# Performance work log

Measured on AMD Instinct MI355X. Metric: run time of the kernel, lower is better.

The kernel has to match this reference:

```python
import jax, jax.numpy as jnp
import numpy as np

NUM_HEADS = 32

def setup_inputs() -> dict:
    key = jax.random.key(0)
    k1, k2, k3 = jax.random.split(key, 3)
    B, C, H, W = 4, 768, 32, 32
    x = jax.random.normal(k1, (B, C, H, W), dtype=jnp.float32)
    # 1x1 conv kernels represented as [C_in, C_out] matrices
    w_qkv = jax.random.normal(k2, (C, 3 * C), dtype=jnp.float32) * (2.0 / (3 * C)) ** 0.5
    b_qkv = jnp.zeros((3 * C,), dtype=jnp.float32)
    w_proj = jax.random.normal(k3, (C, C), dtype=jnp.float32) * (2.0 / C) ** 0.5
    b_proj = jnp.zeros((C,), dtype=jnp.float32)
    return {"x": x, "w_qkv": w_qkv, "b_qkv": b_qkv, "w_proj": w_proj, "b_proj": b_proj}

def reference(x, w_qkv, b_qkv, w_proj, b_proj):
    B, C, H, W = x.shape
    h = NUM_HEADS
    hd = C // h
    scale = hd ** (-0.5)
    # qkv 1x1 conv (channels_first): [B,C,H,W] -> [B,3C,H,W]
    qkv = jnp.einsum('bchw,cd->bdhw', x, w_qkv) + b_qkv[None, :, None, None]
    qkv = qkv.reshape(B, 3, h, hd, H * W)
    q = qkv[:, 0]  # [B,h,hd,HW]
    k = qkv[:, 1]  # [B,h,hd,HW]
    v = qkv[:, 2]  # [B,h,hd,HW]
    # attn = q^T @ k : [B,h,HW,HW]
    attn = jnp.einsum('bhdq,bhdk->bhqk', q, k) * scale
    attn = jax.nn.softmax(attn, axis=-1)
    # out = (attn @ v^T)^T : [B,h,hd,HW]
    o = jnp.einsum('bhqk,bhdk->bhdq', attn, v)
    o = o.reshape(B, C, H, W)
    # proj 1x1 conv
    out = jnp.einsum('bchw,cf->bfhw', o, w_proj) + b_proj[None, :, None, None]
    return out
```

## Files before the change

kernel.cpp:

```cpp
#include <hip/hip_runtime.h>
#include <hip/hip_bf16.h>

#define B_  4
#define C_  768
#define N_  1024
#define NH  32
#define HD  24
#define HDP 32
#define D3  2304
#define QSCALE 0.29448889f

typedef __hip_bfloat16 bf16;
typedef __attribute__((ext_vector_type(8))) short bf16x8;
typedef __attribute__((ext_vector_type(4))) float f32x4;

__device__ __forceinline__ unsigned cvt_pk_bf16(float lo, float hi) {
    unsigned r;
    asm volatile("v_cvt_pk_bf16_f32 %0, %1, %2" : "=v"(r) : "v"(lo), "v"(hi));
    return r;
}

__device__ __forceinline__ float fast_exp2(float x) {
    float r;
    asm volatile("v_exp_f32 %0, %1" : "=v"(r) : "v"(x));
    return r;
}

__device__ __forceinline__ void gload_lds16(const bf16* g, bf16* l) {
    __builtin_amdgcn_global_load_lds(
        (const __attribute__((address_space(1))) void*)g,
        (__attribute__((address_space(3))) void*)l, 16, 0, 0);
}

__global__ __launch_bounds__(256) void transpose_cvt(
        const float* __restrict__ in, bf16* __restrict__ out,
        int R, int Cc, long inb, long outb) {
    __shared__ float tile[32][33];
    const int b = blockIdx.z;
    const float* src = in + (size_t)b * inb;
    bf16* dst = out + (size_t)b * outb;
    const int r0 = blockIdx.y * 32, c0 = blockIdx.x * 32;
    const int tx = threadIdx.x, ty = threadIdx.y;
    #pragma unroll
    for (int k = 0; k < 4; k++)
        tile[ty + 8*k][tx] = src[(size_t)(r0 + ty + 8*k) * Cc + c0 + tx];
    __syncthreads();
    #pragma unroll
    for (int k = 0; k < 4; k++)
        dst[(size_t)(c0 + ty + 8*k) * R + r0 + tx] = __float2bfloat16(tile[tx][ty + 8*k]);
}

__global__ __launch_bounds__(256) void fill_ones(bf16* __restrict__ vB) {
    bf16* row = vB + ((size_t)blockIdx.x * HDP + 24) * N_;
    const ushort4 ones = {0x3F80, 0x3F80, 0x3F80, 0x3F80};
    *(ushort4*)&row[threadIdx.x * 4] = ones;
}

__global__ __launch_bounds__(256) void gemm_qkv(
        const bf16* __restrict__ xt, const bf16* __restrict__ wqT,
        const float* __restrict__ bqkv,
        bf16* __restrict__ qT, bf16* __restrict__ kT, bf16* __restrict__ vB) {
    __shared__ bf16 As[2][128 * 32];
    __shared__ bf16 Bs[2][128 * 32];

    const int b = blockIdx.z;
    const bool vmode = (blockIdx.y >= 12);
    const bf16* Ap; const bf16* Bp; int M0, Nc0;
    if (!vmode) {
        Ap = xt + (size_t)b * N_ * C_;  Bp = wqT;
        M0 = blockIdx.x * 128;          Nc0 = blockIdx.y * 128;
    } else {
        Ap = wqT + (size_t)1536 * C_;   Bp = xt + (size_t)b * N_ * C_;
        M0 = (blockIdx.y - 12) * 128;   Nc0 = blockIdx.x * 128;
    }

    const int t = threadIdx.x;
    const int lane = t & 63, wid = t >> 6;
    const int c = lane & 15, g = lane >> 4;
    const int wm = wid >> 1, wn = wid & 1;

    const int srow = lane >> 2, schunk = lane & 3;
    const bf16* Ag0 = Ap + (size_t)(M0 + wid * 32 + srow) * C_ + schunk * 8;
    const bf16* Ag1 = Ag0 + 16 * C_;
    const bf16* Bg0 = Bp + (size_t)(Nc0 + wid * 32 + srow) * C_ + schunk * 8;
    const bf16* Bg1 = Bg0 + 16 * C_;

    f32x4 acc[4][4];
    #pragma unroll
    for (int i = 0; i < 4; i++)
        #pragma unroll
        for (int j = 0; j < 4; j++) acc[i][j] = f32x4{0.f, 0.f, 0.f, 0.f};

    gload_lds16(Ag0, &As[0][(wid * 32) * 32]);
    gload_lds16(Ag1, &As[0][(wid * 32 + 16) * 32]);
    gload_lds16(Bg0, &Bs[0][(wid * 32) * 32]);
    gload_lds16(Bg1, &Bs[0][(wid * 32 + 16) * 32]);
    __syncthreads();

    int cur = 0;
    for (int s = 0; s < 24; s++) {
        if (s < 23) {
            const int k1 = (s + 1) * 32;
            gload_lds16(Ag0 + k1, &As[cur ^ 1][(wid * 32) * 32]);
            gload_lds16(Ag1 + k1, &As[cur ^ 1][(wid * 32 + 16) * 32]);
            gload_lds16(Bg0 + k1, &Bs[cur ^ 1][(wid * 32) * 32]);
            gload_lds16(Bg1 + k1, &Bs[cur ^ 1][(wid * 32 + 16) * 32]);
        }
        bf16x8 af[4], bfr[4];
        #pragma unroll
        for (int mi = 0; mi < 4; mi++)
            af[mi] = *(const bf16x8*)&As[cur][(wm * 64 + mi * 16 + c) * 32 + g * 8];
        #pragma unroll
        for (int ni = 0; ni < 4; ni++)
            bfr[ni] = *(const bf16x8*)&Bs[cur][(wn * 64 + ni * 16 + c) * 32 + g * 8];
        #pragma unroll
        for (int mi = 0; mi < 4; mi++)
            #pragma unroll
            for (int ni = 0; ni < 4; ni++)
                acc[mi][ni] = __builtin_amdgcn_mfma_f32_16x16x32_bf16(
                    af[mi], bfr[ni], acc[mi][ni], 0, 0, 0);
        __syncthreads();
        cur ^= 1;
    }

    const int row0 = M0 + wm * 64, col0 = Nc0 + wn * 64;
    if (!vmode) {
        #pragma unroll
        for (int ni = 0; ni < 4; ni++) {
            const int j = col0 + ni * 16 + c;
            const int issec = j >= 768;
            bf16* dstbase = issec ? kT : qT;
            const int dd = j - (issec ? 768 : 0);
            const int hh = dd / 24, hd = dd % 24;
            const float bq = bqkv[j];
            const float sca = issec ? 1.0f : QSCALE;
            #pragma unroll
            for (int mi = 0; mi < 4; mi++)
                #pragma unroll
                for (int r = 0; r < 4; r++) {
                    const int n = row0 + mi * 16 + 4 * g + r;
                    dstbase[(((size_t)(b * NH + hh) * N_) + n) * HDP + hd] =
                        __float2bfloat16((acc[mi][ni][r] + bq) * sca);
                }
        }
    } else {
        #pragma unroll
        for (int mi = 0; mi < 4; mi++)
            #pragma unroll
            for (int r = 0; r < 4; r++) {
                const int vd = row0 + mi * 16 + 4 * g + r;
                const int hh = vd / 24, hd = vd % 24;
                const float bq = bqkv[1536 + vd];
                #pragma unroll
                for (int ni = 0; ni < 4; ni++) {
                    const int n = col0 + ni * 16 + c;
                    vB[((size_t)(b * NH + hh) * HDP + hd) * N_ + n] =
                        __float2bfloat16(acc[mi][ni][r] + bq);
                }
            }
    }
}

__global__ __launch_bounds__(256) void gemm_proj(
        const bf16* __restrict__ wpT, const bf16* __restrict__ obuf,
        const float* __restrict__ bproj, float* __restrict__ outF) {
    __shared__ bf16 As[2][64 * 32];
    __shared__ bf16 Bs[2][128 * 32];

    const int b = blockIdx.z;
    const bf16* Ap = wpT;
    const bf16* Bp = obuf + (size_t)b * N_ * C_;
    const int M0 = blockIdx.x * 64, Nc0 = blockIdx.y * 128;

    const int t = threadIdx.x;
    const int lane = t & 63, wid = t >> 6;
    const int c = lane & 15, g = lane >> 4;
    const int wm = wid >> 1, wn = wid & 1;

    const int srow = lane >> 2, schunk = lane & 3;
    const bf16* AgP = Ap + (size_t)(M0 + wid * 16 + srow) * C_ + schunk * 8;
    const bf16* Bg0 = Bp + (size_t)(Nc0 + wid * 32 + srow) * C_ + schunk * 8;
    const bf16* Bg1 = Bg0 + 16 * C_;

    f32x4 acc[2][4];
    #pragma unroll
    for (int i = 0; i < 2; i++)
        #pragma unroll
        for (int j = 0; j < 4; j++) acc[i][j] = f32x4{0.f, 0.f, 0.f, 0.f};

    gload_lds16(AgP, &As[0][(wid * 16) * 32]);
    gload_lds16(Bg0, &Bs[0][(wid * 32) * 32]);
    gload_lds16(Bg1, &Bs[0][(wid * 32 + 16) * 32]);
    __syncthreads();

    int cur = 0;
    for (int s = 0; s < 24; s++) {
        if (s < 23) {
            const int k1 = (s + 1) * 32;
            gload_lds16(AgP + k1, &As[cur ^ 1][(wid * 16) * 32]);
            gload_lds16(Bg0 + k1, &Bs[cur ^ 1][(wid * 32) * 32]);
            gload_lds16(Bg1 + k1, &Bs[cur ^ 1][(wid * 32 + 16) * 32]);
        }
        bf16x8 af[2], bfr[4];
        #pragma unroll
        for (int mi = 0; mi < 2; mi++)
            af[mi] = *(const bf16x8*)&As[cur][(wm * 32 + mi * 16 + c) * 32 + g * 8];
        #pragma unroll
        for (int ni = 0; ni < 4; ni++)
            bfr[ni] = *(const bf16x8*)&Bs[cur][(wn * 64 + ni * 16 + c) * 32 + g * 8];
        #pragma unroll
        for (int mi = 0; mi < 2; mi++)
            #pragma unroll
            for (int ni = 0; ni < 4; ni++)
                acc[mi][ni] = __builtin_amdgcn_mfma_f32_16x16x32_bf16(
                    af[mi], bfr[ni], acc[mi][ni], 0, 0, 0);
        __syncthreads();
        cur ^= 1;
    }

    const int row0 = M0 + wm * 32, col0 = Nc0 + wn * 64;
    #pragma unroll
    for (int mi = 0; mi < 2; mi++)
        #pragma unroll
        for (int r = 0; r < 4; r++) {
            const int f = row0 + mi * 16 + 4 * g + r;
            const float bp = bproj[f];
            #pragma unroll
            for (int ni = 0; ni < 4; ni++) {
                const int n = col0 + ni * 16 + c;
                outF[((size_t)b * C_ + f) * N_ + n] = acc[mi][ni][r] + bp;
            }
        }
}

__global__ __launch_bounds__(256) void attn_mfma(
        const bf16* __restrict__ qT, const bf16* __restrict__ kT,
        const bf16* __restrict__ vB, bf16* __restrict__ obuf) {
    __shared__ bf16 Kb[2][64 * 40];
    __shared__ bf16 Vb[2][32 * 72];
    __shared__ bf16 Ps[4][32 * 72];

    const int t = threadIdx.x, lane = t & 63, wid = t >> 6;
    const int c = lane & 15, g = lane >> 4;
    const int bid = blockIdx.x;
    const int xcd = bid & 7, idx = bid >> 3;
    const int hl = xcd * 16 + (idx & 15);
    const int qb = idx >> 4;
    const int b = hl >> 5, h = hl & 31;
    const int q0 = qb * 128 + wid * 32;
    const size_t hb = (size_t)(b * NH + h);
    const bf16* qh = qT + hb * N_ * HDP;
    const bf16* kh = kT + hb * N_ * HDP;
    const bf16* vh = vB + hb * HDP * N_;
    bf16* myPs = &Ps[wid][0];

    const bf16x8 qf0 = *(const bf16x8*)(qh + (size_t)(q0 + c) * HDP + g * 8);
    const bf16x8 qf1 = *(const bf16x8*)(qh + (size_t)(q0 + 16 + c) * HDP + g * 8);
    f32x4 o00 = {0.f,0.f,0.f,0.f}, o01 = {0.f,0.f,0.f,0.f};
    f32x4 o10 = {0.f,0.f,0.f,0.f}, o11 = {0.f,0.f,0.f,0.f};

    const bf16* kgp = kh + (size_t)(t >> 2) * HDP + (t & 3) * 8;
    const bf16* vgp = vh + (size_t)(t >> 3) * N_ + (t & 7) * 8;
    const int kws = (t >> 2) * 40 + (t & 3) * 8;
    const int vws = (t >> 3) * 72 + (t & 7) * 8;

    int4 rk = *(const int4*)kgp;
    int4 rv = *(const int4*)vgp;
    *(int4*)&Kb[0][kws] = rk;
    *(int4*)&Vb[0][vws] = rv;
    __syncthreads();

    int cur = 0;
    for (int kt = 0; kt < 16; kt++) {
        if (kt < 15) {
            const int k1 = (kt + 1) * 64;
            rk = *(const int4*)(kgp + (size_t)k1 * HDP);
            rv = *(const int4*)(vgp + k1);
        }
        f32x4 st0[4], st1[4];
        #pragma unroll
        for (int tt = 0; tt < 4; tt++) {
            bf16x8 kf = *(const bf16x8*)&Kb[cur][(tt * 16 + c) * 40 + g * 8];
            f32x4 z = {0.f, 0.f, 0.f, 0.f};
            st0[tt] = __builtin_amdgcn_mfma_f32_16x16x32_bf16(kf, qf0, z, 0, 0, 0);
            st1[tt] = __builtin_amdgcn_mfma_f32_16x16x32_bf16(kf, qf1, z, 0, 0, 0);
        }
        float p0[16], p1[16];
        #pragma unroll
        for (int tt = 0; tt < 4; tt++)
            #pragma unroll
            for (int r = 0; r < 4; r++) {
                p0[tt * 4 + r] = fast_exp2(st0[tt][r]);
                p1[tt * 4 + r] = fast_exp2(st1[tt][r]);
            }
        #pragma unroll
        for (int tt = 0; tt < 4; tt++) {
            uint2 w0, w1;
            w0.x = cvt_pk_bf16(p0[tt * 4 + 0], p0[tt * 4 + 1]);
            w0.y = cvt_pk_bf16(p0[tt * 4 + 2], p0[tt * 4 + 3]);
            w1.x = cvt_pk_bf16(p1[tt * 4 + 0], p1[tt * 4 + 1]);
            w1.y = cvt_pk_bf16(p1[tt * 4 + 2], p1[tt * 4 + 3]);
            *(uint2*)&myPs[c * 72 + tt * 16 + g * 4]        = w0;
            *(uint2*)&myPs[(16 + c) * 72 + tt * 16 + g * 4] = w1;
        }
        bf16x8 pa00 = *(const bf16x8*)&myPs[c * 72 + g * 8];
        bf16x8 pa01 = *(const bf16x8*)&myPs[c * 72 + 32 + g * 8];
        bf16x8 pa10 = *(const bf16x8*)&myPs[(16 + c) * 72 + g * 8];
        bf16x8 pa11 = *(const bf16x8*)&myPs[(16 + c) * 72 + 32 + g * 8];

        bf16x8 va0 = *(const bf16x8*)&Vb[cur][c * 72 + g * 8];
        bf16x8 va1 = *(const bf16x8*)&Vb[cur][c * 72 + 32 + g * 8];
        bf16x8 vb0 = *(const bf16x8*)&Vb[cur][(16 + c) * 72 + g * 8];
        bf16x8 vb1 = *(const bf16x8*)&Vb[cur][(16 + c) * 72 + 32 + g * 8];
        o00 = __builtin_amdgcn_mfma_f32_16x16x32_bf16(pa00, va0, o00, 0, 0, 0);
        o00 = __builtin_amdgcn_mfma_f32_16x16x32_bf16(pa01, va1, o00, 0, 0, 0);
        o01 = __builtin_amdgcn_mfma_f32_16x16x32_bf16(pa00, vb0, o01, 0, 0, 0);
        o01 = __builtin_amdgcn_mfma_f32_16x16x32_bf16(pa01, vb1, o01, 0, 0, 0);
        o10 = __builtin_amdgcn_mfma_f32_16x16x32_bf16(pa10, va0, o10, 0, 0, 0);
        o10 = __builtin_amdgcn_mfma_f32_16x16x32_bf16(pa11, va1, o10, 0, 0, 0);
        o11 = __builtin_amdgcn_mfma_f32_16x16x32_bf16(pa10, vb0, o11, 0, 0, 0);
        o11 = __builtin_amdgcn_mfma_f32_16x16x32_bf16(pa11, vb1, o11, 0, 0, 0);

        if (kt < 15) {
            *(int4*)&Kb[cur ^ 1][kws] = rk;
            *(int4*)&Vb[cur ^ 1][vws] = rv;
        }
        __syncthreads();
        cur ^= 1;
    }

    float inv0[4], inv1[4];
    #pragma unroll
    for (int r = 0; r < 4; r++) {
        inv0[r] = 1.f / __shfl(o01[r], g * 16 + 8);
        inv1[r] = 1.f / __shfl(o11[r], g * 16 + 8);
    }
    #pragma unroll
    for (int dt = 0; dt < 2; dt++) {
        const int dcol = dt * 16 + c;
        if (dcol < HD) {
            const f32x4 oa = dt ? o01 : o00;
            const f32x4 ob = dt ? o11 : o10;
            #pragma unroll
            for (int r = 0; r < 4; r++) {
                const int qa = q0 + g * 4 + r;
                const int qb2 = q0 + 16 + g * 4 + r;
                obuf[((size_t)b * N_ + qa) * C_ + h * HD + dcol] =
                    __float2bfloat16(oa[r] * inv0[r]);
                obuf[((size_t)b * N_ + qb2) * C_ + h * HD + dcol] =
                    __float2bfloat16(ob[r] * inv1[r]);
            }
        }
    }
}

extern "C" void kernel_launch(void* const* d_in, const int* in_sizes, int n_in,
                              void* d_out, int out_size, void* d_ws, size_t ws_size,
                              hipStream_t stream) {
    const float* x      = (const float*)d_in[0];
    const float* w_qkv  = (const float*)d_in[1];
    const float* b_qkv  = (const float*)d_in[2];
    const float* w_proj = (const float*)d_in[3];
    const float* b_proj = (const float*)d_in[4];
    float* out = (float*)d_out;

    char* ws = (char*)d_ws;
    bf16* xt   = (bf16*)(ws);
    bf16* wqT  = (bf16*)(ws + 6291456);
    bf16* wpT  = (bf16*)(ws + 9830400);
    bf16* qT   = (bf16*)(ws + 11010048);
    bf16* kT   = (bf16*)(ws + 19398656);
    bf16* vB   = (bf16*)(ws + 27787264);
    bf16* obuf = (bf16*)(ws + 36175872);

    hipMemsetAsync(qT, 0, 8388608, stream);

    transpose_cvt<<<dim3(32, 24, 4), dim3(32, 8), 0, stream>>>(
        x, xt, 768, 1024, (long)768 * 1024, (long)1024 * 768);
    transpose_cvt<<<dim3(72, 24, 1), dim3(32, 8), 0, stream>>>(
        w_qkv, wqT, 768, 2304, 0, 0);
    transpose_cvt<<<dim3(24, 24, 1), dim3(32, 8), 0, stream>>>(
        w_proj, wpT, 768, 768, 0, 0);
    fill_ones<<<dim3(B_ * NH), 256, 0, stream>>>(vB);

    gemm_qkv<<<dim3(8, 18, 4), 256, 0, stream>>>(
        xt, wqT, b_qkv, qT, kT, vB);
    attn_mfma<<<dim3(1024), 256, 0, stream>>>(qT, kT, vB, obuf);
    gemm_proj<<<dim3(12, 8, 4), 256, 0, stream>>>(
        wpT, obuf, b_proj, out);
}
```

Measured before the change: 176.7 us.

## Merge prep kernels, drop qT memset, retile QKV GEMM to 64x128

The three transpose-convert launches and the fill_ones launch become one prep kernel that dispatches on block index, and the hipMemsetAsync on qT is removed. To keep the padded q columns from feeding garbage into attention, the q fragments for lanes g==3 are zeroed in registers instead. The QKV GEMM is flattened to a 1D grid, batch is folded into the M dimension, and the tile shrinks from 128x128 to 64x128 to give more blocks. This aims to cut launch and memset overhead and improve GEMM occupancy, but it relies on the padding columns of K never mattering once q is zeroed.

```diff
diff --git a/kernel.cpp b/kernel.cpp
--- a/kernel.cpp
+++ b/kernel.cpp
@@ -32,15 +32,37 @@
         (__attribute__((address_space(3))) void*)l, 16, 0, 0);
 }
 
-__global__ __launch_bounds__(256) void transpose_cvt(
-        const float* __restrict__ in, bf16* __restrict__ out,
-        int R, int Cc, long inb, long outb) {
+__global__ __launch_bounds__(256) void prep(
+        const float* __restrict__ x, const float* __restrict__ w_qkv,
+        const float* __restrict__ w_proj,
+        bf16* __restrict__ xt, bf16* __restrict__ wqT, bf16* __restrict__ wpT,
+        bf16* __restrict__ vB) {
+    const int bid = blockIdx.x;
+    if (bid >= 5376) {
+        const int head = bid - 5376;
+        bf16* row = vB + ((size_t)head * HDP + 24) * N_;
+        const ushort4 ones = {0x3F80, 0x3F80, 0x3F80, 0x3F80};
+        *(ushort4*)&row[threadIdx.x * 4] = ones;
+        return;
+    }
+    const float* src; bf16* dst; int R, Cc, r0, c0;
+    if (bid < 3072) {
+        const int b = bid / 768, rem = bid % 768;
+        R = 768; Cc = 1024;
+        src = x + (size_t)b * 768 * 1024;
+        dst = xt + (size_t)b * 1024 * 768;
+        c0 = (rem % 32) * 32; r0 = (rem / 32) * 32;
+    } else if (bid < 4800) {
+        const int rem = bid - 3072;
+        R = 768; Cc = 2304; src = w_qkv; dst = wqT;
+        c0 = (rem % 72) * 32; r0 = (rem / 72) * 32;
+    } else {
+        const int rem = bid - 4800;
+        R = 768; Cc = 768; src = w_proj; dst = wpT;
+        c0 = (rem % 24) * 32; r0 = (rem / 24) * 32;
+    }
     __shared__ float tile[32][33];
-    const int b = blockIdx.z;
-    const float* src = in + (size_t)b * inb;
-    bf16* dst = out + (size_t)b * outb;
-    const int r0 = blockIdx.y * 32, c0 = blockIdx.x * 32;
-    const int tx = threadIdx.x, ty = threadIdx.y;
+    const int tx = threadIdx.x & 31, ty = threadIdx.x >> 5;
     #pragma unroll
     for (int k = 0; k < 4; k++)
         tile[ty + 8*k][tx] = src[(size_t)(r0 + ty + 8*k) * Cc + c0 + tx];
@@ -48,30 +70,25 @@
     #pragma unroll
     for (int k = 0; k < 4; k++)
         dst[(size_t)(c0 + ty + 8*k) * R + r0 + tx] = __float2bfloat16(tile[tx][ty + 8*k]);
-}
-
-__global__ __launch_bounds__(256) void fill_ones(bf16* __restrict__ vB) {
-    bf16* row = vB + ((size_t)blockIdx.x * HDP + 24) * N_;
-    const ushort4 ones = {0x3F80, 0x3F80, 0x3F80, 0x3F80};
-    *(ushort4*)&row[threadIdx.x * 4] = ones;
 }
 
 __global__ __launch_bounds__(256) void gemm_qkv(
         const bf16* __restrict__ xt, const bf16* __restrict__ wqT,
         const float* __restrict__ bqkv,
         bf16* __restrict__ qT, bf16* __restrict__ kT, bf16* __restrict__ vB) {
-    __shared__ bf16 As[2][128 * 32];
+    __shared__ bf16 As[2][64 * 32];
     __shared__ bf16 Bs[2][128 * 32];
 
-    const int b = blockIdx.z;
-    const bool vmode = (blockIdx.y >= 12);
+    const int bid = blockIdx.x;
+    const bool vmode = (bid >= 768);
     const bf16* Ap; const bf16* Bp; int M0, Nc0;
     if (!vmode) {
-        Ap = xt + (size_t)b * N_ * C_;  Bp = wqT;
-        M0 = blockIdx.x * 128;          Nc0 = blockIdx.y * 128;
+        Ap = xt;                       Bp = wqT;
+        M0 = (bid & 63) * 64;          Nc0 = (bid >> 6) * 128;
     } else {
-        Ap = wqT + (size_t)1536 * C_;   Bp = xt + (size_t)b * N_ * C_;
-        M0 = (blockIdx.y - 12) * 128;   Nc0 = blockIdx.x * 128;
+        const int r = bid - 768;
+        Ap = wqT + (size_t)1536 * C_;  Bp = xt;
+        M0 = (r % 12) * 64;            Nc0 = (r / 12) * 128;
     }
 
     const int t = threadIdx.x;
@@ -80,19 +97,17 @@
     const int wm = wid >> 1, wn = wid & 1;
 
     const int srow = lane >> 2, schunk = lane & 3;
-    const bf16* Ag0 = Ap + (size_t)(M0 + wid * 32 + srow) * C_ + schunk * 8;
-    const bf16* Ag1 = Ag0 + 16 * C_;
+    const bf16* AgP = Ap + (size_t)(M0 + wid * 16 + srow) * C_ + schunk * 8;
     const bf16* Bg0 = Bp + (size_t)(Nc0 + wid * 32 + srow) * C_ + schunk * 8;
     const bf16* Bg1 = Bg0 + 16 * C_;
 
-    f32x4 acc[4][4];
-    #pragma unroll
-    for (int i = 0; i < 4; i++)
+    f32x4 acc[2][4];
+    #pragma unroll
+    for (int i = 0; i < 2; i++)
         #pragma unroll
         for (int j = 0; j < 4; j++) acc[i][j] = f32x4{0.f, 0.f, 0.f, 0.f};
 
-    gload_lds16(Ag0, &As[0][(wid * 32) * 32]);
-    gload_lds16(Ag1, &As[0][(wid * 32 + 16) * 32]);
+    gload_lds16(AgP, &As[0][(wid * 16) * 32]);
     gload_lds16(Bg0, &Bs[0][(wid * 32) * 32]);
     gload_lds16(Bg1, &Bs[0][(wid * 32 + 16) * 32]);
     __syncthreads();
@@ -101,20 +116,19 @@
     for (int s = 0; s < 24; s++) {
         if (s < 23) {
             const int k1 = (s + 1) * 32;
-            gload_lds16(Ag0 + k1, &As[cur ^ 1][(wid * 32) * 32]);
-            gload_lds16(Ag1 + k1, &As[cur ^ 1][(wid * 32 + 16) * 32]);
+            gload_lds16(AgP + k1, &As[cur ^ 1][(wid * 16) * 32]);
             gload_lds16(Bg0 + k1, &Bs[cur ^ 1][(wid * 32) * 32]);
             gload_lds16(Bg1 + k1, &Bs[cur ^ 1][(wid * 32 + 16) * 32]);
         }
-        bf16x8 af[4], bfr[4];
-        #pragma unroll
-        for (int mi = 0; mi < 4; mi++)
-            af[mi] = *(const bf16x8*)&As[cur][(wm * 64 + mi * 16 + c) * 32 + g * 8];
+        bf16x8 af[2], bfr[4];
+        #pragma unroll
+        for (int mi = 0; mi < 2; mi++)
+            af[mi] = *(const bf16x8*)&As[cur][(wm * 32 + mi * 16 + c) * 32 + g * 8];
         #pragma unroll
         for (int ni = 0; ni < 4; ni++)
             bfr[ni] = *(const bf16x8*)&Bs[cur][(wn * 64 + ni * 16 + c) * 32 + g * 8];
         #pragma unroll
-        for (int mi = 0; mi < 4; mi++)
+        for (int mi = 0; mi < 2; mi++)
             #pragma unroll
             for (int ni = 0; ni < 4; ni++)
                 acc[mi][ni] = __builtin_amdgcn_mfma_f32_16x16x32_bf16(
@@ -123,7 +137,7 @@
         cur ^= 1;
     }
 
-    const int row0 = M0 + wm * 64, col0 = Nc0 + wn * 64;
+    const int row0 = M0 + wm * 32, col0 = Nc0 + wn * 64;
     if (!vmode) {
         #pragma unroll
         for (int ni = 0; ni < 4; ni++) {
@@ -135,17 +149,18 @@
             const float bq = bqkv[j];
             const float sca = issec ? 1.0f : QSCALE;
             #pragma unroll
-            for (int mi = 0; mi < 4; mi++)
+            for (int mi = 0; mi < 2; mi++)
                 #pragma unroll
                 for (int r = 0; r < 4; r++) {
                     const int n = row0 + mi * 16 + 4 * g + r;
-                    dstbase[(((size_t)(b * NH + hh) * N_) + n) * HDP + hd] =
+                    const int b = n >> 10, nn = n & 1023;
+                    dstbase[(((size_t)(b * NH + hh) * N_) + nn) * HDP + hd] =
                         __float2bfloat16((acc[mi][ni][r] + bq) * sca);
                 }
         }
     } else {
         #pragma unroll
-        for (int mi = 0; mi < 4; mi++)
+        for (int mi = 0; mi < 2; mi++)
             #pragma unroll
             for (int r = 0; r < 4; r++) {
                 const int vd = row0 + mi * 16 + 4 * g + r;
@@ -154,7 +169,8 @@
                 #pragma unroll
                 for (int ni = 0; ni < 4; ni++) {
                     const int n = col0 + ni * 16 + c;
-                    vB[((size_t)(b * NH + hh) * HDP + hd) * N_ + n] =
+                    const int b = n >> 10, nn = n & 1023;
+                    vB[((size_t)(b * NH + hh) * HDP + hd) * N_ + nn] =
                         __float2bfloat16(acc[mi][ni][r] + bq);
                 }
             }
@@ -254,8 +270,12 @@
     const bf16* vh = vB + hb * HDP * N_;
     bf16* myPs = &Ps[wid][0];
 
-    const bf16x8 qf0 = *(const bf16x8*)(qh + (size_t)(q0 + c) * HDP + g * 8);
-    const bf16x8 qf1 = *(const bf16x8*)(qh + (size_t)(q0 + 16 + c) * HDP + g * 8);
+    bf16x8 qf0 = *(const bf16x8*)(qh + (size_t)(q0 + c) * HDP + g * 8);
+    bf16x8 qf1 = *(const bf16x8*)(qh + (size_t)(q0 + 16 + c) * HDP + g * 8);
+    if (g == 3) {
+        const bf16x8 z8 = {0, 0, 0, 0, 0, 0, 0, 0};
+        qf0 = z8; qf1 = z8;
+    }
     f32x4 o00 = {0.f,0.f,0.f,0.f}, o01 = {0.f,0.f,0.f,0.f};
     f32x4 o10 = {0.f,0.f,0.f,0.f}, o11 = {0.f,0.f,0.f,0.f};
 
@@ -373,19 +393,8 @@
     bf16* vB   = (bf16*)(ws + 27787264);
     bf16* obuf = (bf16*)(ws + 36175872);
 
-    hipMemsetAsync(qT, 0, 8388608, stream);
-
-    transpose_cvt<<<dim3(32, 24, 4), dim3(32, 8), 0, stream>>>(
-        x, xt, 768, 1024, (long)768 * 1024, (long)1024 * 768);
-    transpose_cvt<<<dim3(72, 24, 1), dim3(32, 8), 0, stream>>>(
-        w_qkv, wqT, 768, 2304, 0, 0);
-    transpose_cvt<<<dim3(24, 24, 1), dim3(32, 8), 0, stream>>>(
-        w_proj, wpT, 768, 768, 0, 0);
-    fill_ones<<<dim3(B_ * NH), 256, 0, stream>>>(vB);
-
-    gemm_qkv<<<dim3(8, 18, 4), 256, 0, stream>>>(
-        xt, wqT, b_qkv, qT, kT, vB);
+    prep<<<dim3(5504), 256, 0, stream>>>(x, w_qkv, w_proj, xt, wqT, wpT, vB);
+    gemm_qkv<<<dim3(1152), 256, 0, stream>>>(xt, wqT, b_qkv, qT, kT, vB);
     attn_mfma<<<dim3(1024), 256, 0, stream>>>(qT, kT, vB, obuf);
-    gemm_proj<<<dim3(12, 8, 4), 256, 0, stream>>>(
-        wpT, obuf, b_proj, out);
-}
+    gemm_proj<<<dim3(12, 8, 4), 256, 0, stream>>>(wpT, obuf, b_proj, out);
+}
```

Result: faster. 166.0 us (-6.0%).
